# Kernel tuning notes

Hardware: AMD Instinct MI355X
Metric: run time of the kernel (lower is better)

The kernel has to match this reference:

```python
import jax, jax.numpy as jnp
import numpy as np

N_NODES = 10000
N_EDGES = 320000
N_GRAPHS = 64


def _seg_max0(data, seg, num_segments):
    # segment max; empty segments get 0 (matches PyG scatter-max fill behavior)
    agg = jax.ops.segment_max(data, seg, num_segments=num_segments)
    return jnp.where(jnp.isneginf(agg), 0.0, agg)


def _edge_conv(x, src, dst, W, b, n_nodes):
    # PyG EdgeConv: message = nn(cat([x_i, x_j - x_i])), aggr='max' at target i
    xi = x[dst]                       # [E, d]
    xj = x[src]                       # [E, d]
    m = jax.nn.sigmoid(jnp.concatenate([xi, xj - xi], axis=-1) @ W + b)  # [E, d_out]
    return _seg_max0(m, dst, n_nodes)


def setup_inputs() -> dict:
    key = jax.random.key(0)
    ks = jax.random.split(key, 12)
    x = jax.random.normal(ks[0], (N_NODES, 3), dtype=jnp.float32)
    edge_index = jax.random.randint(ks[1], (2, N_EDGES), 0, N_NODES, dtype=jnp.int64)
    batch = jnp.sort(jax.random.randint(ks[2], (N_NODES,), 0, N_GRAPHS, dtype=jnp.int64))

    def lin(k, fan_in, fan_out):
        kw, kb = jax.random.split(k)
        lim = 1.0 / np.sqrt(fan_in)
        W = jax.random.uniform(kw, (fan_in, fan_out), jnp.float32, -lim, lim)
        b = jax.random.uniform(kb, (fan_out,), jnp.float32, -lim, lim)
        return W, b

    W1, b1 = lin(ks[3], 6, 128)     # EdgeConv1 MLP: Linear(2*3, 128)
    W2, b2 = lin(ks[4], 256, 256)   # EdgeConv2 MLP: Linear(2*128, 256)
    W3, b3 = lin(ks[5], 256, 128)   # output Linear(256, 128)
    W4, b4 = lin(ks[6], 128, 10)    # output Linear(128, output_classes)
    return {"x": x, "edge_index": edge_index, "batch": batch,
            "W1": W1, "b1": b1, "W2": W2, "b2": b2,
            "W3": W3, "b3": b3, "W4": W4, "b4": b4}


def reference(x, edge_index, batch, W1, b1, W2, b2, W3, b3, W4, b4):
    src, dst = edge_index[0], edge_index[1]
    h = _edge_conv(x, src, dst, W1, b1, N_NODES)    # [N, 128]
    h = _edge_conv(h, src, dst, W2, b2, N_NODES)    # [N, 256]
    g = _seg_max0(h, batch, N_GRAPHS)               # [G, 256] graph max-pool
    out = jax.nn.sigmoid(g @ W3 + b3) @ W4 + b4     # [G, 10]
    return out
```

## Files before the change

### kernel.cpp

```cpp
#include <hip/hip_runtime.h>

#define N_NODES  10000
#define N_EDGES  320000
#define N_GRAPHS 64

#define RB 1250
#define RP 313
#define RW 256

typedef __attribute__((ext_vector_type(8))) __bf16 bf16x8;
typedef __attribute__((ext_vector_type(4))) float f32x4;
typedef __attribute__((ext_vector_type(4))) unsigned int u32x4;

__device__ __forceinline__ float sigm(float z) { return 1.0f / (1.0f + __expf(-z)); }

__device__ __forceinline__ unsigned short f2bf(float f) {
    unsigned int u = __float_as_uint(f);
    return (unsigned short)((u + 0x7fffu + ((u >> 16) & 1u)) >> 16);
}
__device__ __forceinline__ float bf2f(unsigned short h) { return __uint_as_float(((unsigned int)h) << 16); }
__device__ __forceinline__ float bflo(unsigned int u) { return __uint_as_float(u << 16); }
__device__ __forceinline__ float bfhi(unsigned int u) { return __uint_as_float(u & 0xffff0000u); }

__global__ __launch_bounds__(256) void prep_k(
        const unsigned int* __restrict__ ei_raw, const unsigned int* __restrict__ b_raw,
        const float* __restrict__ x, const float* __restrict__ W1, const float* __restrict__ b1,
        const float* __restrict__ W2,
        int* __restrict__ src, int* __restrict__ dst, int* __restrict__ bat,
        int* __restrict__ deg, float* __restrict__ P1, unsigned short* __restrict__ Q1,
        unsigned short* __restrict__ Bh, unsigned short* __restrict__ Bl,
        float* __restrict__ g) {
    int bx = blockIdx.x, t = threadIdx.x;
    if (bx < RB) {
        __shared__ int snz[2];
        if (t < 2) snz[t] = 0;
        __syncthreads();
        {
            unsigned int wv = ei_raw[bx * 512 + 2 * t + 1];
            unsigned long long m = __ballot(wv != 0);
            if ((t & 63) == 0 && m) atomicAdd(&snz[0], __popcll(m));
        }
        if (bx * 256 < N_NODES) {
            int w0 = min(bx * 512, N_NODES - 512);
            unsigned int bv = b_raw[w0 + 2 * t + 1];
            unsigned long long m = __ballot(bv != 0);
            if ((t & 63) == 0 && m) atomicAdd(&snz[1], __popcll(m));
        }
        __syncthreads();
        int i = bx * 256 + t;
        int i32e = snz[0] > 16;
        const int* ei = (const int*)ei_raw;
        if (i < N_EDGES) {
            int s = i32e ? ei[i] : ei[2 * i];
            int d = i32e ? ei[N_EDGES + i] : ei[2 * (N_EDGES + i)];
            src[i] = s;
            dst[i] = d;
            atomicAdd(&deg[d], 1);
        }
        if (i < N_NODES) {
            int i32b = snz[1] > 16;
            const int* bb = (const int*)b_raw;
            bat[i] = i32b ? bb[i] : bb[2 * i];
        }
    } else if (bx < RB + RP) {
        __shared__ float xs[96];
        int c = t;
        float k0, k1, k2, bias;
        if (c < 128) {
            k0 = W1[0 * 128 + c] - W1[3 * 128 + c];
            k1 = W1[1 * 128 + c] - W1[4 * 128 + c];
            k2 = W1[2 * 128 + c] - W1[5 * 128 + c];
            bias = b1[c];
        } else {
            int cc = c - 128;
            k0 = W1[3 * 128 + cc];
            k1 = W1[4 * 128 + cc];
            k2 = W1[5 * 128 + cc];
            bias = 0.f;
        }
        int n0 = (bx - RB) * 32;
        int nmax = min(32, N_NODES - n0);
        if (t < 96) xs[t] = (t < nmax * 3) ? x[n0 * 3 + t] : 0.f;
        __syncthreads();
        for (int tt = 0; tt < nmax; tt++) {
            float v = bias + xs[tt * 3 + 0] * k0 + xs[tt * 3 + 1] * k1 + xs[tt * 3 + 2] * k2;
            if (c < 128) P1[(n0 + tt) * 128 + c] = v;
            else         Q1[(n0 + tt) * 128 + (c - 128)] = f2bf(v);
        }
    } else if (bx < RB + RP + RW) {
        int idx = (bx - RB - RP) * 256 + t;
        int nn = idx >> 7, k = idx & 127;
        float wc;
        if (nn < 256) wc = W2[k * 256 + nn] - W2[(128 + k) * 256 + nn];
        else          wc = W2[(128 + k) * 256 + (nn - 256)];
        unsigned short h = f2bf(wc);
        Bh[idx] = h;
        Bl[idx] = f2bf(wc - bf2f(h));
    } else {
        float4 z = make_float4(0.f, 0.f, 0.f, 0.f);
#pragma unroll
        for (int it = 0; it < 16; it++) *(float4*)&g[(t + it * 256) * 4] = z;
    }
}

__global__ void scan_k(const int* __restrict__ deg, int* __restrict__ offs,
                       int* __restrict__ cursor, int n) {
    __shared__ int wsum[16];
    int t = threadIdx.x;
    int base = t * 10;
    int v[10];
    int run = 0;
#pragma unroll
    for (int k = 0; k < 10; k++) {
        int i = base + k;
        int d = (i < n) ? deg[i] : 0;
        v[k] = run;
        run += d;
    }
    int lane = t & 63;
    int incl = run;
#pragma unroll
    for (int d = 1; d < 64; d <<= 1) {
        int u = __shfl_up(incl, d);
        if (lane >= d) incl += u;
    }
    if (lane == 63) wsum[t >> 6] = incl;
    __syncthreads();
    if (t < 16) {
        int s = wsum[t];
#pragma unroll
        for (int d = 1; d < 16; d <<= 1) {
            int u = __shfl_up(s, d, 16);
            if (t >= d) s += u;
        }
        wsum[t] = s;
    }
    __syncthreads();
    int wbase = (t >> 6) ? wsum[(t >> 6) - 1] : 0;
    int excl = wbase + incl - run;
#pragma unroll
    for (int k = 0; k < 10; k++) {
        int i = base + k;
        if (i < n) { int o = excl + v[k]; offs[i] = o; cursor[i] = o; }
    }
    if (t == 1023) offs[n] = wsum[15];
}

__global__ void scatter_k(const int* __restrict__ src, const int* __restrict__ dst,
                          int* __restrict__ cursor, int* __restrict__ csr, int E) {
    int e = blockIdx.x * blockDim.x + threadIdx.x;
    if (e < E) {
        int pos = atomicAdd(&cursor[dst[e]], 1);
        csr[pos] = src[e];
    }
}

__global__ void econv1_k(const float* __restrict__ P1, const unsigned int* __restrict__ Q1u,
                         const int* __restrict__ offs, const int* __restrict__ csr,
                         unsigned short* __restrict__ h1h, unsigned short* __restrict__ h1l) {
    int i = blockIdx.x;
    int c = threadIdx.x;
    int s = offs[i], e = offs[i + 1];
    float o0 = 0.f, o1 = 0.f;
    if (e > s) {
        float z0 = -3.4e38f, z1 = -3.4e38f;
        int k = s;
        for (; k + 3 < e; k += 4) {
            int j0 = csr[k], j1 = csr[k + 1], j2 = csr[k + 2], j3 = csr[k + 3];
            unsigned int u0 = Q1u[j0 * 64 + c];
            unsigned int u1 = Q1u[j1 * 64 + c];
            unsigned int u2 = Q1u[j2 * 64 + c];
            unsigned int u3 = Q1u[j3 * 64 + c];
            z0 = fmaxf(z0, fmaxf(fmaxf(bflo(u0), bflo(u1)), fmaxf(bflo(u2), bflo(u3))));
            z1 = fmaxf(z1, fmaxf(fmaxf(bfhi(u0), bfhi(u1)), fmaxf(bfhi(u2), bfhi(u3))));
        }
        for (; k < e; k++) {
            unsigned int u = Q1u[csr[k] * 64 + c];
            z0 = fmaxf(z0, bflo(u));
            z1 = fmaxf(z1, bfhi(u));
        }
        unsigned long long pv =
            __builtin_nontemporal_load((const unsigned long long*)&P1[i * 128 + 2 * c]);
        float px = __uint_as_float((unsigned int)pv);
        float py = __uint_as_float((unsigned int)(pv >> 32));
        o0 = sigm(px + z0);
        o1 = sigm(py + z1);
    }
    unsigned short hh0 = f2bf(o0), hh1 = f2bf(o1);
    unsigned short hl0 = f2bf(o0 - bf2f(hh0)), hl1 = f2bf(o1 - bf2f(hh1));
    *(ushort2*)&h1h[i * 128 + 2 * c] = make_ushort2(hh0, hh1);
    *(ushort2*)&h1l[i * 128 + 2 * c] = make_ushort2(hl0, hl1);
}

__global__ __launch_bounds__(256) void gemm2_k(
        const unsigned short* __restrict__ Ahg, const unsigned short* __restrict__ Alg,
        const unsigned short* __restrict__ Bhg, const unsigned short* __restrict__ Blg,
        const float* __restrict__ b2, float* __restrict__ P2,
        unsigned short* __restrict__ Q2, int n) {
    __shared__ __align__(16) char smem[65536];
    char* Ahb = smem;
    char* Alb = smem + 16384;
    char* Bhb = smem + 32768;
    char* Blb = smem + 49152;
    int t = threadIdx.x;
    int m0 = blockIdx.x * 64;
    int n0 = blockIdx.y * 64;
#pragma unroll
    for (int it = 0; it < 4; it++) {
        int c = t + it * 256;
        int row = c >> 4, kb = c & 15;
        int dsa = (row * 256 + kb * 16) ^ ((row & 7) << 4);
        u32x4 va = {0u, 0u, 0u, 0u}, vl = {0u, 0u, 0u, 0u};
        if (m0 + row < n) {
            va = *(const u32x4*)&Ahg[(m0 + row) * 128 + kb * 8];
            vl = *(const u32x4*)&Alg[(m0 + row) * 128 + kb * 8];
        }
        *(u32x4*)(Ahb + dsa) = va;
        *(u32x4*)(Alb + dsa) = vl;
        *(u32x4*)(Bhb + dsa) = *(const u32x4*)&Bhg[(n0 + row) * 128 + kb * 8];
        *(u32x4*)(Blb + dsa) = *(const u32x4*)&Blg[(n0 + row) * 128 + kb * 8];
    }
    __syncthreads();

    int w = t >> 6, lane = t & 63;
    int lr = lane & 15, lg = lane >> 4;
    int am = 16 * w + lr;
    int abase = am * 256 + lg * 16;
    int asw = (am & 7) << 4;
    bf16x8 ah[4], al[4];
#pragma unroll
    for (int kk = 0; kk < 4; kk++) {
        int off = (abase + kk * 64) ^ asw;
        ah[kk] = *(const bf16x8*)(Ahb + off);
        al[kk] = *(const bf16x8*)(Alb + off);
    }
    int bsw = (lr & 7) << 4;
#pragma unroll
    for (int nt = 0; nt < 4; nt++) {
        int nb = (nt * 16 + lr) * 256 + lg * 16;
        f32x4 acc = {0.f, 0.f, 0.f, 0.f};
#pragma unroll
        for (int kk = 0; kk < 4; kk++) {
            int off = (nb + kk * 64) ^ bsw;
            bf16x8 bh = *(const bf16x8*)(Bhb + off);
            bf16x8 bl = *(const bf16x8*)(Blb + off);
            acc = __builtin_amdgcn_mfma_f32_16x16x32_bf16(ah[kk], bh, acc, 0, 0, 0);
            acc = __builtin_amdgcn_mfma_f32_16x16x32_bf16(al[kk], bh, acc, 0, 0, 0);
            acc = __builtin_amdgcn_mfma_f32_16x16x32_bf16(ah[kk], bl, acc, 0, 0, 0);
        }
        int colg = n0 + nt * 16 + lr;
        int mbase = m0 + 16 * w + 4 * lg;
        if (colg < 256) {
            float bias = b2[colg];
#pragma unroll
            for (int r = 0; r < 4; r++) {
                int m = mbase + r;
                if (m < n)
                    __builtin_nontemporal_store(acc[r] + bias, &P2[(size_t)m * 256 + colg]);
            }
        } else {
            int qc = colg - 256;
#pragma unroll
            for (int r = 0; r < 4; r++) {
                int m = mbase + r;
                if (m < n) Q2[(size_t)m * 256 + qc] = f2bf(acc[r]);
            }
        }
    }
}

__global__ void econv2_k(const float* __restrict__ P2, const unsigned int* __restrict__ Q2u,
                         const int* __restrict__ offs, const int* __restrict__ csr,
                         const int* __restrict__ bat, float* __restrict__ g) {
    int i = blockIdx.x;
    int s = offs[i], e = offs[i + 1];
    if (s == e) return;
    int cc = blockIdx.y * 64 + threadIdx.x;
    float z0 = -3.4e38f, z1 = -3.4e38f;
    int k = s;
    for (; k + 3 < e; k += 4) {
        int j0 = csr[k], j1 = csr[k + 1], j2 = csr[k + 2], j3 = csr[k + 3];
        unsigned int u0 = Q2u[(size_t)j0 * 128 + cc];
        unsigned int u1 = Q2u[(size_t)j1 * 128 + cc];
        unsigned int u2 = Q2u[(size_t)j2 * 128 + cc];
        unsigned int u3 = Q2u[(size_t)j3 * 128 + cc];
        z0 = fmaxf(z0, fmaxf(fmaxf(bflo(u0), bflo(u1)), fmaxf(bflo(u2), bflo(u3))));
        z1 = fmaxf(z1, fmaxf(fmaxf(bfhi(u0), bfhi(u1)), fmaxf(bfhi(u2), bfhi(u3))));
    }
    for (; k < e; k++) {
        unsigned int u = Q2u[(size_t)csr[k] * 128 + cc];
        z0 = fmaxf(z0, bflo(u));
        z1 = fmaxf(z1, bfhi(u));
    }
    unsigned long long pv =
        __builtin_nontemporal_load((const unsigned long long*)&P2[(size_t)i * 256 + 2 * cc]);
    float px = __uint_as_float((unsigned int)pv);
    float py = __uint_as_float((unsigned int)(pv >> 32));
    float h0 = sigm(px + z0);
    float h1 = sigm(py + z1);
    int gb = bat[i] * 256 + 2 * cc;
    atomicMax((unsigned int*)&g[gb + 0], __float_as_uint(h0));
    atomicMax((unsigned int*)&g[gb + 1], __float_as_uint(h1));
}

__global__ void final_k(const float* __restrict__ g, const float* __restrict__ W3,
                        const float* __restrict__ b3, const float* __restrict__ W4,
                        const float* __restrict__ b4, float* __restrict__ out) {
    __shared__ float gs[256];
    __shared__ float ss[128];
    int b = blockIdx.x, t = threadIdx.x;
    gs[t] = g[b * 256 + t];
    gs[t + 128] = g[b * 256 + 128 + t];
    __syncthreads();
    float acc = b3[t];
#pragma unroll 8
    for (int k = 0; k < 256; k++) acc += gs[k] * W3[k * 128 + t];
    ss[t] = sigm(acc);
    __syncthreads();
    if (t < 10) {
        float o = b4[t];
#pragma unroll 8
        for (int k = 0; k < 128; k++) o += ss[k] * W4[k * 10 + t];
        out[b * 10 + t] = o;
    }
}

extern "C" void kernel_launch(void* const* d_in, const int* in_sizes, int n_in,
                              void* d_out, int out_size, void* d_ws, size_t ws_size,
                              hipStream_t stream) {
    const float* x  = (const float*)d_in[0];
    const void*  ei_raw = d_in[1];
    const void*  b_raw  = d_in[2];
    const float* W1 = (const float*)d_in[3];
    const float* b1 = (const float*)d_in[4];
    const float* W2 = (const float*)d_in[5];
    const float* b2 = (const float*)d_in[6];
    const float* W3 = (const float*)d_in[7];
    const float* b3 = (const float*)d_in[8];
    const float* W4 = (const float*)d_in[9];
    const float* b4 = (const float*)d_in[10];

    char* ws = (char*)d_ws;
    size_t off = 0;
    auto alloc = [&](size_t bytes) {
        void* p = ws + off;
        off += (bytes + 255) & ~(size_t)255;
        return p;
    };
    int*            src    = (int*)alloc(N_EDGES * 4);
    int*            dst    = (int*)alloc(N_EDGES * 4);
    int*            bat    = (int*)alloc(N_NODES * 4);
    int*            deg    = (int*)alloc(N_NODES * 4);
    int*            offs   = (int*)alloc((N_NODES + 1) * 4);
    int*            cursor = (int*)alloc(N_NODES * 4);
    int*            csr    = (int*)alloc(N_EDGES * 4);
    float*          P1     = (float*)alloc((size_t)N_NODES * 128 * 4);
    unsigned short* Q1     = (unsigned short*)alloc((size_t)N_NODES * 128 * 2);
    unsigned short* h1h    = (unsigned short*)alloc((size_t)N_NODES * 128 * 2);
    unsigned short* h1l    = (unsigned short*)alloc((size_t)N_NODES * 128 * 2);
    unsigned short* Bh     = (unsigned short*)alloc(512 * 128 * 2);
    unsigned short* Bl     = (unsigned short*)alloc(512 * 128 * 2);
    float*          P2     = (float*)alloc((size_t)N_NODES * 256 * 4);
    unsigned short* Q2     = (unsigned short*)alloc((size_t)N_NODES * 256 * 2);
    float*          g      = (float*)alloc(N_GRAPHS * 256 * 4);

    hipMemsetAsync(deg, 0, N_NODES * 4, stream);

    prep_k<<<RB + RP + RW + 1, 256, 0, stream>>>(
        (const unsigned int*)ei_raw, (const unsigned int*)b_raw, x, W1, b1, W2,
        src, dst, bat, deg, P1, Q1, Bh, Bl, g);
    scan_k<<<1, 1024, 0, stream>>>(deg, offs, cursor, N_NODES);
    scatter_k<<<(N_EDGES + 255) / 256, 256, 0, stream>>>(src, dst, cursor, csr, N_EDGES);

    econv1_k<<<N_NODES, 64, 0, stream>>>(P1, (const unsigned int*)Q1, offs, csr, h1h, h1l);
    gemm2_k<<<dim3((N_NODES + 63) / 64, 8), 256, 0, stream>>>(h1h, h1l, Bh, Bl, b2, P2, Q2, N_NODES);

    econv2_k<<<dim3(N_NODES, 2), 64, 0, stream>>>(P2, (const unsigned int*)Q2, offs, csr, bat, g);
    final_k<<<N_GRAPHS, 128, 0, stream>>>(g, W3, b3, W4, b4, (float*)d_out);
}
```

Baseline: 211.8 us.

## Replace atomic graph max-pool with segmented pool kernel and wave-per-node gathers

The second edge-conv kernel now writes per-node outputs to a new fp32 buffer instead of doing atomicMax into the graph pool. A new pool kernel then reduces each graph's contiguous node range, with graph boundaries found by binary search in the scan kernel. This removes the atomics and the zero-init of the pool buffer. Both gather kernels also switch to four waves per 256-thread block and load neighbor indices once per wave, broadcasting them with shuffles instead of each lane re-reading csr. The cost is an extra ~10 MB write and read of h2 plus a small 128-block pool kernel that walks about 156 nodes serially per graph.

Result: slower. 223.1 us (+5.3%).

```diff
diff --git a/kernel.cpp b/kernel.cpp
--- a/kernel.cpp
+++ b/kernel.cpp
@@ -28,8 +28,7 @@
         const float* __restrict__ W2,
         int* __restrict__ src, int* __restrict__ dst, int* __restrict__ bat,
         int* __restrict__ deg, float* __restrict__ P1, unsigned short* __restrict__ Q1,
-        unsigned short* __restrict__ Bh, unsigned short* __restrict__ Bl,
-        float* __restrict__ g) {
+        unsigned short* __restrict__ Bh, unsigned short* __restrict__ Bl) {
     int bx = blockIdx.x, t = threadIdx.x;
     if (bx < RB) {
         __shared__ int snz[2];
@@ -87,7 +86,7 @@
             if (c < 128) P1[(n0 + tt) * 128 + c] = v;
             else         Q1[(n0 + tt) * 128 + (c - 128)] = f2bf(v);
         }
-    } else if (bx < RB + RP + RW) {
+    } else {
         int idx = (bx - RB - RP) * 256 + t;
         int nn = idx >> 7, k = idx & 127;
         float wc;
@@ -96,15 +95,12 @@
         unsigned short h = f2bf(wc);
         Bh[idx] = h;
         Bl[idx] = f2bf(wc - bf2f(h));
-    } else {
-        float4 z = make_float4(0.f, 0.f, 0.f, 0.f);
-#pragma unroll
-        for (int it = 0; it < 16; it++) *(float4*)&g[(t + it * 256) * 4] = z;
-    }
-}
-
-__global__ void scan_k(const int* __restrict__ deg, int* __restrict__ offs,
-                       int* __restrict__ cursor, int n) {
+    }
+}
+
+__global__ void scan_k(const int* __restrict__ deg, const int* __restrict__ bat,
+                       int* __restrict__ offs, int* __restrict__ cursor,
+                       int* __restrict__ gstart, int n) {
     __shared__ int wsum[16];
     int t = threadIdx.x;
     int base = t * 10;
@@ -144,6 +140,14 @@
         if (i < n) { int o = excl + v[k]; offs[i] = o; cursor[i] = o; }
     }
     if (t == 1023) offs[n] = wsum[15];
+    if (t < N_GRAPHS + 1) {
+        int lo = 0, hi = n;
+        while (lo < hi) {
+            int mid = (lo + hi) >> 1;
+            if (bat[mid] < t) lo = mid + 1; else hi = mid;
+        }
+        gstart[t] = lo;
+    }
 }
 
 __global__ void scatter_k(const int* __restrict__ src, const int* __restrict__ dst,
@@ -155,32 +159,39 @@
     }
 }
 
-__global__ void econv1_k(const float* __restrict__ P1, const unsigned int* __restrict__ Q1u,
-                         const int* __restrict__ offs, const int* __restrict__ csr,
-                         unsigned short* __restrict__ h1h, unsigned short* __restrict__ h1l) {
-    int i = blockIdx.x;
-    int c = threadIdx.x;
+__global__ __launch_bounds__(256) void econv1_k(
+        const float* __restrict__ P1, const unsigned int* __restrict__ Q1u,
+        const int* __restrict__ offs, const int* __restrict__ csr,
+        unsigned short* __restrict__ h1h, unsigned short* __restrict__ h1l) {
+    int lane = threadIdx.x & 63;
+    int i = blockIdx.x * 4 + (threadIdx.x >> 6);
+    if (i >= N_NODES) return;
     int s = offs[i], e = offs[i + 1];
     float o0 = 0.f, o1 = 0.f;
     if (e > s) {
         float z0 = -3.4e38f, z1 = -3.4e38f;
-        int k = s;
-        for (; k + 3 < e; k += 4) {
-            int j0 = csr[k], j1 = csr[k + 1], j2 = csr[k + 2], j3 = csr[k + 3];
-            unsigned int u0 = Q1u[j0 * 64 + c];
-            unsigned int u1 = Q1u[j1 * 64 + c];
-            unsigned int u2 = Q1u[j2 * 64 + c];
-            unsigned int u3 = Q1u[j3 * 64 + c];
-            z0 = fmaxf(z0, fmaxf(fmaxf(bflo(u0), bflo(u1)), fmaxf(bflo(u2), bflo(u3))));
-            z1 = fmaxf(z1, fmaxf(fmaxf(bfhi(u0), bfhi(u1)), fmaxf(bfhi(u2), bfhi(u3))));
-        }
-        for (; k < e; k++) {
-            unsigned int u = Q1u[csr[k] * 64 + c];
-            z0 = fmaxf(z0, bflo(u));
-            z1 = fmaxf(z1, bfhi(u));
+        for (int base = s; base < e; base += 64) {
+            int cnt = min(64, e - base);
+            int jv = (lane < cnt) ? csr[base + lane] : 0;
+            int j = 0;
+            for (; j + 3 < cnt; j += 4) {
+                int j0 = __shfl(jv, j), j1 = __shfl(jv, j + 1);
+                int j2 = __shfl(jv, j + 2), j3 = __shfl(jv, j + 3);
+                unsigned int u0 = Q1u[j0 * 64 + lane];
+                unsigned int u1 = Q1u[j1 * 64 + lane];
+                unsigned int u2 = Q1u[j2 * 64 + lane];
+                unsigned int u3 = Q1u[j3 * 64 + lane];
+                z0 = fmaxf(z0, fmaxf(fmaxf(bflo(u0), bflo(u1)), fmaxf(bflo(u2), bflo(u3))));
+                z1 = fmaxf(z1, fmaxf(fmaxf(bfhi(u0), bfhi(u1)), fmaxf(bfhi(u2), bfhi(u3))));
+            }
+            for (; j < cnt; j++) {
+                unsigned int u = Q1u[__shfl(jv, j) * 64 + lane];
+                z0 = fmaxf(z0, bflo(u));
+                z1 = fmaxf(z1, bfhi(u));
+            }
         }
         unsigned long long pv =
-            __builtin_nontemporal_load((const unsigned long long*)&P1[i * 128 + 2 * c]);
+            __builtin_nontemporal_load((const unsigned long long*)&P1[i * 128 + 2 * lane]);
         float px = __uint_as_float((unsigned int)pv);
         float py = __uint_as_float((unsigned int)(pv >> 32));
         o0 = sigm(px + z0);
@@ -188,8 +199,8 @@
     }
     unsigned short hh0 = f2bf(o0), hh1 = f2bf(o1);
     unsigned short hl0 = f2bf(o0 - bf2f(hh0)), hl1 = f2bf(o1 - bf2f(hh1));
-    *(ushort2*)&h1h[i * 128 + 2 * c] = make_ushort2(hh0, hh1);
-    *(ushort2*)&h1l[i * 128 + 2 * c] = make_ushort2(hl0, hl1);
+    *(ushort2*)&h1h[i * 128 + 2 * lane] = make_ushort2(hh0, hh1);
+    *(ushort2*)&h1l[i * 128 + 2 * lane] = make_ushort2(hl0, hl1);
 }
 
 __global__ __launch_bounds__(256) void gemm2_k(
@@ -269,38 +280,70 @@
     }
 }
 
-__global__ void econv2_k(const float* __restrict__ P2, const unsigned int* __restrict__ Q2u,
-                         const int* __restrict__ offs, const int* __restrict__ csr,
-                         const int* __restrict__ bat, float* __restrict__ g) {
-    int i = blockIdx.x;
+__global__ __launch_bounds__(256) void econv2_k(
+        const float* __restrict__ P2, const unsigned int* __restrict__ Q2u,
+        const int* __restrict__ offs, const int* __restrict__ csr,
+        float* __restrict__ h2) {
+    int lane = threadIdx.x & 63;
+    int p = blockIdx.x * 4 + (threadIdx.x >> 6);
+    int i = p >> 1, half = p & 1;
+    if (i >= N_NODES) return;
+    int cc = half * 64 + lane;
     int s = offs[i], e = offs[i + 1];
-    if (s == e) return;
-    int cc = blockIdx.y * 64 + threadIdx.x;
-    float z0 = -3.4e38f, z1 = -3.4e38f;
-    int k = s;
-    for (; k + 3 < e; k += 4) {
-        int j0 = csr[k], j1 = csr[k + 1], j2 = csr[k + 2], j3 = csr[k + 3];
-        unsigned int u0 = Q2u[(size_t)j0 * 128 + cc];
-        unsigned int u1 = Q2u[(size_t)j1 * 128 + cc];
-        unsigned int u2 = Q2u[(size_t)j2 * 128 + cc];
-        unsigned int u3 = Q2u[(size_t)j3 * 128 + cc];
-        z0 = fmaxf(z0, fmaxf(fmaxf(bflo(u0), bflo(u1)), fmaxf(bflo(u2), bflo(u3))));
-        z1 = fmaxf(z1, fmaxf(fmaxf(bfhi(u0), bfhi(u1)), fmaxf(bfhi(u2), bfhi(u3))));
-    }
-    for (; k < e; k++) {
-        unsigned int u = Q2u[(size_t)csr[k] * 128 + cc];
-        z0 = fmaxf(z0, bflo(u));
-        z1 = fmaxf(z1, bfhi(u));
-    }
-    unsigned long long pv =
-        __builtin_nontemporal_load((const unsigned long long*)&P2[(size_t)i * 256 + 2 * cc]);
-    float px = __uint_as_float((unsigned int)pv);
-    float py = __uint_as_float((unsigned int)(pv >> 32));
-    float h0 = sigm(px + z0);
-    float h1 = sigm(py + z1);
-    int gb = bat[i] * 256 + 2 * cc;
-    atomicMax((unsigned int*)&g[gb + 0], __float_as_uint(h0));
-    atomicMax((unsigned int*)&g[gb + 1], __float_as_uint(h1));
+    float2 o = make_float2(0.f, 0.f);
+    if (e > s) {
+        float z0 = -3.4e38f, z1 = -3.4e38f;
+        for (int base = s; base < e; base += 64) {
+            int cnt = min(64, e - base);
+            int jv = (lane < cnt) ? csr[base + lane] : 0;
+            int j = 0;
+            for (; j + 3 < cnt; j += 4) {
+                int j0 = __shfl(jv, j), j1 = __shfl(jv, j + 1);
+                int j2 = __shfl(jv, j + 2), j3 = __shfl(jv, j + 3);
+                unsigned int u0 = Q2u[(size_t)j0 * 128 + cc];
+                unsigned int u1 = Q2u[(size_t)j1 * 128 + cc];
+                unsigned int u2 = Q2u[(size_t)j2 * 128 + cc];
+                unsigned int u3 = Q2u[(size_t)j3 * 128 + cc];
+                z0 = fmaxf(z0, fmaxf(fmaxf(bflo(u0), bflo(u1)), fmaxf(bflo(u2), bflo(u3))));
+                z1 = fmaxf(z1, fmaxf(fmaxf(bfhi(u0), bfhi(u1)), fmaxf(bfhi(u2), bfhi(u3))));
+            }
+            for (; j < cnt; j++) {
+                unsigned int u = Q2u[(size_t)__shfl(jv, j) * 128 + cc];
+                z0 = fmaxf(z0, bflo(u));
+                z1 = fmaxf(z1, bfhi(u));
+            }
+        }
+        unsigned long long pv =
+            __builtin_nontemporal_load((const unsigned long long*)&P2[(size_t)i * 256 + 2 * cc]);
+        float px = __uint_as_float((unsigned int)pv);
+        float py = __uint_as_float((unsigned int)(pv >> 32));
+        o.x = sigm(px + z0);
+        o.y = sigm(py + z1);
+    }
+    *(float2*)&h2[(size_t)i * 256 + 2 * cc] = o;
+}
+
+__global__ void pool_k(const float* __restrict__ h2, const int* __restrict__ gstart,
+                       float* __restrict__ g) {
+    int gi = blockIdx.x;
+    int col = blockIdx.y * 128 + 2 * threadIdx.x;
+    int s = gstart[gi], e = gstart[gi + 1];
+    float m0 = 0.f, m1 = 0.f;
+    int i = s;
+    for (; i + 3 < e; i += 4) {
+        float2 a = *(const float2*)&h2[(size_t)(i + 0) * 256 + col];
+        float2 b = *(const float2*)&h2[(size_t)(i + 1) * 256 + col];
+        float2 c = *(const float2*)&h2[(size_t)(i + 2) * 256 + col];
+        float2 d = *(const float2*)&h2[(size_t)(i + 3) * 256 + col];
+        m0 = fmaxf(m0, fmaxf(fmaxf(a.x, b.x), fmaxf(c.x, d.x)));
+        m1 = fmaxf(m1, fmaxf(fmaxf(a.y, b.y), fmaxf(c.y, d.y)));
+    }
+    for (; i < e; i++) {
+        float2 a = *(const float2*)&h2[(size_t)i * 256 + col];
+        m0 = fmaxf(m0, a.x);
+        m1 = fmaxf(m1, a.y);
+    }
+    *(float2*)&g[gi * 256 + col] = make_float2(m0, m1);
 }
 
 __global__ void final_k(const float* __restrict__ g, const float* __restrict__ W3,
@@ -354,6 +397,7 @@
     int*            offs   = (int*)alloc((N_NODES + 1) * 4);
     int*            cursor = (int*)alloc(N_NODES * 4);
     int*            csr    = (int*)alloc(N_EDGES * 4);
+    int*            gstart = (int*)alloc((N_GRAPHS + 1) * 4);
     float*          P1     = (float*)alloc((size_t)N_NODES * 128 * 4);
     unsigned short* Q1     = (unsigned short*)alloc((size_t)N_NODES * 128 * 2);
     unsigned short* h1h    = (unsigned short*)alloc((size_t)N_NODES * 128 * 2);
@@ -362,19 +406,21 @@
     unsigned short* Bl     = (unsigned short*)alloc(512 * 128 * 2);
     float*          P2     = (float*)alloc((size_t)N_NODES * 256 * 4);
     unsigned short* Q2     = (unsigned short*)alloc((size_t)N_NODES * 256 * 2);
+    float*          h2     = (float*)alloc((size_t)N_NODES * 256 * 4);
     float*          g      = (float*)alloc(N_GRAPHS * 256 * 4);
 
     hipMemsetAsync(deg, 0, N_NODES * 4, stream);
 
-    prep_k<<<RB + RP + RW + 1, 256, 0, stream>>>(
+    prep_k<<<RB + RP + RW, 256, 0, stream>>>(
         (const unsigned int*)ei_raw, (const unsigned int*)b_raw, x, W1, b1, W2,
-        src, dst, bat, deg, P1, Q1, Bh, Bl, g);
-    scan_k<<<1, 1024, 0, stream>>>(deg, offs, cursor, N_NODES);
+        src, dst, bat, deg, P1, Q1, Bh, Bl);
+    scan_k<<<1, 1024, 0, stream>>>(deg, bat, offs, cursor, gstart, N_NODES);
     scatter_k<<<(N_EDGES + 255) / 256, 256, 0, stream>>>(src, dst, cursor, csr, N_EDGES);
 
-    econv1_k<<<N_NODES, 64, 0, stream>>>(P1, (const unsigned int*)Q1, offs, csr, h1h, h1l);
+    econv1_k<<<(N_NODES + 3) / 4, 256, 0, stream>>>(P1, (const unsigned int*)Q1, offs, csr, h1h, h1l);
     gemm2_k<<<dim3((N_NODES + 63) / 64, 8), 256, 0, stream>>>(h1h, h1l, Bh, Bl, b2, P2, Q2, N_NODES);
 
-    econv2_k<<<dim3(N_NODES, 2), 64, 0, stream>>>(P2, (const unsigned int*)Q2, offs, csr, bat, g);
+    econv2_k<<<(2 * N_NODES + 3) / 4, 256, 0, stream>>>(P2, (const unsigned int*)Q2, offs, csr, h2);
+    pool_k<<<dim3(N_GRAPHS, 2), 64, 0, stream>>>(h2, gstart, g);
     final_k<<<N_GRAPHS, 128, 0, stream>>>(g, W3, b3, W4, b4, (float*)d_out);
 }
```

## Use 16-bit edge indices and pack four nodes per block in econv kernels

Applied to the files above, without the earlier changes.

Edge source/destination arrays and the CSR neighbor list are stored as 16-bit indices instead of 32-bit, since node ids fit below 65536. This halves index traffic in the scatter and gather kernels. The econv kernels now launch 256-thread blocks covering four nodes each, one wavefront per node. econv2 has each lane handle four channels through 8-byte loads, so the two channel-halves no longer re-read the CSR list and offsets separately. The 16-bit indices hard-code the assumption that node ids stay below 65536.

After: 228.9 us. 1.08x slower.

```diff
diff --git a/kernel.cpp b/kernel.cpp
--- a/kernel.cpp
+++ b/kernel.cpp
@@ -26,8 +26,9 @@
         const unsigned int* __restrict__ ei_raw, const unsigned int* __restrict__ b_raw,
         const float* __restrict__ x, const float* __restrict__ W1, const float* __restrict__ b1,
         const float* __restrict__ W2,
-        int* __restrict__ src, int* __restrict__ dst, int* __restrict__ bat,
-        int* __restrict__ deg, float* __restrict__ P1, unsigned short* __restrict__ Q1,
+        unsigned short* __restrict__ src16, unsigned short* __restrict__ dst16,
+        int* __restrict__ bat, int* __restrict__ deg,
+        float* __restrict__ P1, unsigned short* __restrict__ Q1,
         unsigned short* __restrict__ Bh, unsigned short* __restrict__ Bl,
         float* __restrict__ g) {
     int bx = blockIdx.x, t = threadIdx.x;
@@ -53,8 +54,8 @@
         if (i < N_EDGES) {
             int s = i32e ? ei[i] : ei[2 * i];
             int d = i32e ? ei[N_EDGES + i] : ei[2 * (N_EDGES + i)];
-            src[i] = s;
-            dst[i] = d;
+            src16[i] = (unsigned short)s;
+            dst16[i] = (unsigned short)d;
             atomicAdd(&deg[d], 1);
         }
         if (i < N_NODES) {
@@ -146,20 +147,24 @@
     if (t == 1023) offs[n] = wsum[15];
 }
 
-__global__ void scatter_k(const int* __restrict__ src, const int* __restrict__ dst,
-                          int* __restrict__ cursor, int* __restrict__ csr, int E) {
+__global__ void scatter_k(const unsigned short* __restrict__ src16,
+                          const unsigned short* __restrict__ dst16,
+                          int* __restrict__ cursor, unsigned short* __restrict__ csr, int E) {
     int e = blockIdx.x * blockDim.x + threadIdx.x;
     if (e < E) {
-        int pos = atomicAdd(&cursor[dst[e]], 1);
-        csr[pos] = src[e];
-    }
-}
-
-__global__ void econv1_k(const float* __restrict__ P1, const unsigned int* __restrict__ Q1u,
-                         const int* __restrict__ offs, const int* __restrict__ csr,
-                         unsigned short* __restrict__ h1h, unsigned short* __restrict__ h1l) {
-    int i = blockIdx.x;
-    int c = threadIdx.x;
+        int d = dst16[e];
+        int pos = atomicAdd(&cursor[d], 1);
+        csr[pos] = src16[e];
+    }
+}
+
+__global__ __launch_bounds__(256) void econv1_k(
+        const float* __restrict__ P1, const unsigned int* __restrict__ Q1u,
+        const int* __restrict__ offs, const unsigned short* __restrict__ csr,
+        unsigned short* __restrict__ h1h, unsigned short* __restrict__ h1l) {
+    int lane = threadIdx.x & 63;
+    int i = blockIdx.x * 4 + (threadIdx.x >> 6);
+    if (i >= N_NODES) return;
     int s = offs[i], e = offs[i + 1];
     float o0 = 0.f, o1 = 0.f;
     if (e > s) {
@@ -167,20 +172,20 @@
         int k = s;
         for (; k + 3 < e; k += 4) {
             int j0 = csr[k], j1 = csr[k + 1], j2 = csr[k + 2], j3 = csr[k + 3];
-            unsigned int u0 = Q1u[j0 * 64 + c];
-            unsigned int u1 = Q1u[j1 * 64 + c];
-            unsigned int u2 = Q1u[j2 * 64 + c];
-            unsigned int u3 = Q1u[j3 * 64 + c];
+            unsigned int u0 = Q1u[j0 * 64 + lane];
+            unsigned int u1 = Q1u[j1 * 64 + lane];
+            unsigned int u2 = Q1u[j2 * 64 + lane];
+            unsigned int u3 = Q1u[j3 * 64 + lane];
             z0 = fmaxf(z0, fmaxf(fmaxf(bflo(u0), bflo(u1)), fmaxf(bflo(u2), bflo(u3))));
             z1 = fmaxf(z1, fmaxf(fmaxf(bfhi(u0), bfhi(u1)), fmaxf(bfhi(u2), bfhi(u3))));
         }
         for (; k < e; k++) {
-            unsigned int u = Q1u[csr[k] * 64 + c];
+            unsigned int u = Q1u[csr[k] * 64 + lane];
             z0 = fmaxf(z0, bflo(u));
             z1 = fmaxf(z1, bfhi(u));
         }
         unsigned long long pv =
-            __builtin_nontemporal_load((const unsigned long long*)&P1[i * 128 + 2 * c]);
+            __builtin_nontemporal_load((const unsigned long long*)&P1[i * 128 + 2 * lane]);
         float px = __uint_as_float((unsigned int)pv);
         float py = __uint_as_float((unsigned int)(pv >> 32));
         o0 = sigm(px + z0);
@@ -188,8 +193,8 @@
     }
     unsigned short hh0 = f2bf(o0), hh1 = f2bf(o1);
     unsigned short hl0 = f2bf(o0 - bf2f(hh0)), hl1 = f2bf(o1 - bf2f(hh1));
-    *(ushort2*)&h1h[i * 128 + 2 * c] = make_ushort2(hh0, hh1);
-    *(ushort2*)&h1l[i * 128 + 2 * c] = make_ushort2(hl0, hl1);
+    *(ushort2*)&h1h[i * 128 + 2 * lane] = make_ushort2(hh0, hh1);
+    *(ushort2*)&h1l[i * 128 + 2 * lane] = make_ushort2(hl0, hl1);
 }
 
 __global__ __launch_bounds__(256) void gemm2_k(
@@ -269,38 +274,41 @@
     }
 }
 
-__global__ void econv2_k(const float* __restrict__ P2, const unsigned int* __restrict__ Q2u,
-                         const int* __restrict__ offs, const int* __restrict__ csr,
-                         const int* __restrict__ bat, float* __restrict__ g) {
-    int i = blockIdx.x;
+__global__ __launch_bounds__(256) void econv2_k(
+        const float* __restrict__ P2, const unsigned int* __restrict__ Q2u,
+        const int* __restrict__ offs, const unsigned short* __restrict__ csr,
+        const int* __restrict__ bat, float* __restrict__ g) {
+    int lane = threadIdx.x & 63;
+    int i = blockIdx.x * 4 + (threadIdx.x >> 6);
+    if (i >= N_NODES) return;
     int s = offs[i], e = offs[i + 1];
-    if (s == e) return;
-    int cc = blockIdx.y * 64 + threadIdx.x;
-    float z0 = -3.4e38f, z1 = -3.4e38f;
+    if (e == s) return;
+    float z0 = -3.4e38f, z1 = -3.4e38f, z2 = -3.4e38f, z3 = -3.4e38f;
     int k = s;
     for (; k + 3 < e; k += 4) {
         int j0 = csr[k], j1 = csr[k + 1], j2 = csr[k + 2], j3 = csr[k + 3];
-        unsigned int u0 = Q2u[(size_t)j0 * 128 + cc];
-        unsigned int u1 = Q2u[(size_t)j1 * 128 + cc];
-        unsigned int u2 = Q2u[(size_t)j2 * 128 + cc];
-        unsigned int u3 = Q2u[(size_t)j3 * 128 + cc];
-        z0 = fmaxf(z0, fmaxf(fmaxf(bflo(u0), bflo(u1)), fmaxf(bflo(u2), bflo(u3))));
-        z1 = fmaxf(z1, fmaxf(fmaxf(bfhi(u0), bfhi(u1)), fmaxf(bfhi(u2), bfhi(u3))));
+        uint2 u0 = *(const uint2*)&Q2u[(size_t)j0 * 128 + 2 * lane];
+        uint2 u1 = *(const uint2*)&Q2u[(size_t)j1 * 128 + 2 * lane];
+        uint2 u2 = *(const uint2*)&Q2u[(size_t)j2 * 128 + 2 * lane];
+        uint2 u3 = *(const uint2*)&Q2u[(size_t)j3 * 128 + 2 * lane];
+        z0 = fmaxf(z0, fmaxf(fmaxf(bflo(u0.x), bflo(u1.x)), fmaxf(bflo(u2.x), bflo(u3.x))));
+        z1 = fmaxf(z1, fmaxf(fmaxf(bfhi(u0.x), bfhi(u1.x)), fmaxf(bfhi(u2.x), bfhi(u3.x))));
+        z2 = fmaxf(z2, fmaxf(fmaxf(bflo(u0.y), bflo(u1.y)), fmaxf(bflo(u2.y), bflo(u3.y))));
+        z3 = fmaxf(z3, fmaxf(fmaxf(bfhi(u0.y), bfhi(u1.y)), fmaxf(bfhi(u2.y), bfhi(u3.y))));
     }
     for (; k < e; k++) {
-        unsigned int u = Q2u[(size_t)csr[k] * 128 + cc];
-        z0 = fmaxf(z0, bflo(u));
-        z1 = fmaxf(z1, bfhi(u));
-    }
-    unsigned long long pv =
-        __builtin_nontemporal_load((const unsigned long long*)&P2[(size_t)i * 256 + 2 * cc]);
-    float px = __uint_as_float((unsigned int)pv);
-    float py = __uint_as_float((unsigned int)(pv >> 32));
-    float h0 = sigm(px + z0);
-    float h1 = sigm(py + z1);
-    int gb = bat[i] * 256 + 2 * cc;
-    atomicMax((unsigned int*)&g[gb + 0], __float_as_uint(h0));
-    atomicMax((unsigned int*)&g[gb + 1], __float_as_uint(h1));
+        uint2 u = *(const uint2*)&Q2u[(size_t)csr[k] * 128 + 2 * lane];
+        z0 = fmaxf(z0, bflo(u.x));
+        z1 = fmaxf(z1, bfhi(u.x));
+        z2 = fmaxf(z2, bflo(u.y));
+        z3 = fmaxf(z3, bfhi(u.y));
+    }
+    f32x4 p = __builtin_nontemporal_load((const f32x4*)&P2[(size_t)i * 256 + 4 * lane]);
+    int gb = bat[i] * 256 + 4 * lane;
+    atomicMax((unsigned int*)&g[gb + 0], __float_as_uint(sigm(p.x + z0)));
+    atomicMax((unsigned int*)&g[gb + 1], __float_as_uint(sigm(p.y + z1)));
+    atomicMax((unsigned int*)&g[gb + 2], __float_as_uint(sigm(p.z + z2)));
+    atomicMax((unsigned int*)&g[gb + 3], __float_as_uint(sigm(p.w + z3)));
 }
 
 __global__ void final_k(const float* __restrict__ g, const float* __restrict__ W3,
@@ -347,13 +355,13 @@
         off += (bytes + 255) & ~(size_t)255;
         return p;
     };
-    int*            src    = (int*)alloc(N_EDGES * 4);
-    int*            dst    = (int*)alloc(N_EDGES * 4);
+    unsigned short* src16  = (unsigned short*)alloc(N_EDGES * 2);
+    unsigned short* dst16  = (unsigned short*)alloc(N_EDGES * 2);
     int*            bat    = (int*)alloc(N_NODES * 4);
     int*            deg    = (int*)alloc(N_NODES * 4);
     int*            offs   = (int*)alloc((N_NODES + 1) * 4);
     int*            cursor = (int*)alloc(N_NODES * 4);
-    int*            csr    = (int*)alloc(N_EDGES * 4);
+    unsigned short* csr    = (unsigned short*)alloc(N_EDGES * 2);
     float*          P1     = (float*)alloc((size_t)N_NODES * 128 * 4);
     unsigned short* Q1     = (unsigned short*)alloc((size_t)N_NODES * 128 * 2);
     unsigned short* h1h    = (unsigned short*)alloc((size_t)N_NODES * 128 * 2);
@@ -368,13 +376,13 @@
 
     prep_k<<<RB + RP + RW + 1, 256, 0, stream>>>(
         (const unsigned int*)ei_raw, (const unsigned int*)b_raw, x, W1, b1, W2,
-        src, dst, bat, deg, P1, Q1, Bh, Bl, g);
+        src16, dst16, bat, deg, P1, Q1, Bh, Bl, g);
     scan_k<<<1, 1024, 0, stream>>>(deg, offs, cursor, N_NODES);
-    scatter_k<<<(N_EDGES + 255) / 256, 256, 0, stream>>>(src, dst, cursor, csr, N_EDGES);
-
-    econv1_k<<<N_NODES, 64, 0, stream>>>(P1, (const unsigned int*)Q1, offs, csr, h1h, h1l);
+    scatter_k<<<(N_EDGES + 255) / 256, 256, 0, stream>>>(src16, dst16, cursor, csr, N_EDGES);
+
+    econv1_k<<<(N_NODES + 3) / 4, 256, 0, stream>>>(P1, (const unsigned int*)Q1, offs, csr, h1h, h1l);
     gemm2_k<<<dim3((N_NODES + 63) / 64, 8), 256, 0, stream>>>(h1h, h1l, Bh, Bl, b2, P2, Q2, N_NODES);
 
-    econv2_k<<<dim3(N_NODES, 2), 64, 0, stream>>>(P2, (const unsigned int*)Q2, offs, csr, bat, g);
+    econv2_k<<<(N_NODES + 3) / 4, 256, 0, stream>>>(P2, (const unsigned int*)Q2, offs, csr, bat, g);
     final_k<<<N_GRAPHS, 128, 0, stream>>>(g, W3, b3, W4, b4, (float*)d_out);
 }
```
